# Kernel tuning notes

Hardware: AMD Instinct MI355X
Metric: run time of the kernel (lower is better)

## Reference

```python
import jax, jax.numpy as jnp
import numpy as np

DIM = 1024
NUM_HEADS = 16
HEAD_DIM = DIM // NUM_HEADS
SCALE = HEAD_DIM ** -0.5


def setup_inputs() -> dict:
    key = jax.random.key(0)
    k1, k2, k3 = jax.random.split(key, 3)
    x = jax.random.normal(k1, (4, 2048, DIM), dtype=jnp.float32)
    w_qkv = jax.random.normal(k2, (DIM, 3 * DIM), dtype=jnp.float32) * (DIM ** -0.5)
    b_qkv = jnp.zeros((3 * DIM,), dtype=jnp.float32)
    w_proj = jax.random.normal(k3, (DIM, DIM), dtype=jnp.float32) * (DIM ** -0.5)
    b_proj = jnp.zeros((DIM,), dtype=jnp.float32)
    return {"x": x, "w_qkv": w_qkv, "b_qkv": b_qkv, "w_proj": w_proj, "b_proj": b_proj}


def reference(x, w_qkv, b_qkv, w_proj, b_proj):
    b, n, c = x.shape
    qkv = x @ w_qkv + b_qkv                       # [b, n, 3*dim]
    qkv = qkv.reshape(b, n, 3, NUM_HEADS, HEAD_DIM)
    qkv = jnp.transpose(qkv, (2, 0, 3, 1, 4))     # [3, b, H, n, hd]
    q, k, v = qkv[0], qkv[1], qkv[2]
    attn = jnp.einsum("bhqd,bhkd->bhqk", q, k) * SCALE
    attn = jax.nn.softmax(attn, axis=-1)
    out = jnp.einsum("bhqk,bhkd->bhqd", attn, v)  # [b, H, n, hd]
    out = jnp.transpose(out, (0, 2, 1, 3)).reshape(b, n, c)
    return out @ w_proj + b_proj
```

## Files before the change

### kernel.cpp

```cpp
#include <hip/hip_runtime.h>
#include <hip/hip_bf16.h>

typedef unsigned short u16;
typedef __attribute__((ext_vector_type(8))) short bf16x8;
typedef __attribute__((ext_vector_type(4))) float f32x4;
typedef __attribute__((ext_vector_type(16))) float f32x16;


__device__ __forceinline__ u16 f2bf(float f) {
  union { float f; unsigned u; } v; v.f = f;
  unsigned r = v.u + 0x7fffu + ((v.u >> 16) & 1u);
  return (u16)(r >> 16);
}

#if defined(__has_builtin)
#if __has_builtin(__builtin_amdgcn_cvt_pk_bf16_f32)
#define HAS_PK_BF16 1
#endif
#endif
__device__ __forceinline__ unsigned pk2bf(float a, float b) {
#ifdef HAS_PK_BF16
  typedef __attribute__((ext_vector_type(2))) __bf16 vbf2;
  union { vbf2 v; unsigned u; } u;
  u.v = __builtin_amdgcn_cvt_pk_bf16_f32(a, b);
  return u.u;
#else
  return (unsigned)f2bf(a) | ((unsigned)f2bf(b) << 16);
#endif
}

__device__ __forceinline__ f32x4 mfma16(bf16x8 a, bf16x8 b, f32x4 c) {
  return __builtin_amdgcn_mfma_f32_16x16x32_bf16(a, b, c, 0, 0, 0);
}
__device__ __forceinline__ f32x16 mfma32(bf16x8 a, bf16x8 b, f32x16 c) {
  return __builtin_amdgcn_mfma_f32_32x32x16_bf16(a, b, c, 0, 0, 0);
}

__device__ __forceinline__ void gl_lds16(const void* g, void* l) {
  __builtin_amdgcn_global_load_lds((__attribute__((address_space(1))) void*)g,
                                   (__attribute__((address_space(3))) void*)l,
                                   16, 0, 0);
}


__global__ void cvt_f32_bf16(const float* __restrict__ in, u16* __restrict__ out, int n) {
  int i = (blockIdx.x * blockDim.x + threadIdx.x) * 4;
  if (i >= n) return;
  float4 v = *(const float4*)(in + i);
  u16 o0 = f2bf(v.x), o1 = f2bf(v.y), o2 = f2bf(v.z), o3 = f2bf(v.w);
  ushort4 o; o.x = o0; o.y = o1; o.z = o2; o.w = o3;
  *(ushort4*)(out + i) = o;
}

__global__ void transpose_cvt2(const float* __restrict__ wq, const float* __restrict__ wp,
                               u16* __restrict__ oq, u16* __restrict__ op) {
  __shared__ u16 tile[64][65];
  const int bx = blockIdx.x;
  const float* in; u16* out; int C, c0;
  if (bx < 48) { in = wq; out = oq; C = 3072; c0 = bx * 64; }
  else         { in = wp; out = op; C = 1024; c0 = (bx - 48) * 64; }
  const int R = 1024;
  int r0 = blockIdx.y * 64;
  int lc = threadIdx.x & 63, lr = threadIdx.x >> 6;
#pragma unroll
  for (int i = 0; i < 16; ++i) {
    int r = lr + i * 4;
    tile[r][lc] = f2bf(in[(size_t)(r0 + r) * C + c0 + lc]);
  }
  __syncthreads();
#pragma unroll
  for (int i = 0; i < 16; ++i) {
    int c = lr + i * 4;
    out[(size_t)(c0 + c) * R + r0 + lc] = tile[lc][c];
  }
}


struct Smem128 { u16 A0[8192]; u16 B0[16384]; u16 A1[8192]; u16 B1[16384]; };

#define LDB128(base, off) (*(const bf16x8*)((const char*)(base) + (off)))
#define ISSUE_A(dst, j, k0) \
  gl_lds16(pA + (size_t)(j) * 32768 + (k0), (dst) + (j) * 4096 + dsel)
#define ISSUE_B(dst, j, k0) \
  gl_lds16(pB + (size_t)(j) * 65536 + (k0), (dst) + (j) * 4096 + dsel)

#define KSTEP(CA, CB, NA, NB, k0n, PF)                                         \
  do {                                                                         \
    bf16x8 aL[2][2], aH[2][2], bL[2][2], bH[2][2];                             \
            \
    _Pragma("unroll") for (int mt = 0; mt < 2; ++mt) {                         \
      aL[mt][0] = LDB128(CA, aoff + mt * 2048 + cp0);                          \
      aL[mt][1] = LDB128(CA, aoff + mt * 2048 + cp1);                          \
    }                                                                          \
    _Pragma("unroll") for (int nt = 0; nt < 2; ++nt) {                         \
      bL[nt][0] = LDB128(CB, boff + nt * 2048 + cp0);                          \
      bL[nt][1] = LDB128(CB, boff + nt * 2048 + cp1);                          \
    }                                                                          \
    if (PF) { ISSUE_B(NB, 0, k0n); ISSUE_B(NB, 1, k0n); }                      \
    __builtin_amdgcn_s_setprio(1);                                             \
    _Pragma("unroll") for (int mt = 0; mt < 2; ++mt)                           \
      _Pragma("unroll") for (int nt = 0; nt < 2; ++nt) {                       \
        acc[mt][nt] = mfma16(aL[mt][0], bL[nt][0], acc[mt][nt]);               \
        acc[mt][nt] = mfma16(aL[mt][1], bL[nt][1], acc[mt][nt]);               \
      }                                                                        \
    __builtin_amdgcn_s_setprio(0);                                             \
                          \
    _Pragma("unroll") for (int nt = 0; nt < 2; ++nt) {                         \
      bH[nt][0] = LDB128(CB, boff + (nt + 2) * 2048 + cp0);                    \
      bH[nt][1] = LDB128(CB, boff + (nt + 2) * 2048 + cp1);                    \
    }                                                                          \
    if (PF) { ISSUE_B(NB, 2, k0n); ISSUE_B(NB, 3, k0n); ISSUE_A(NA, 0, k0n); } \
    __builtin_amdgcn_s_setprio(1);                                             \
    _Pragma("unroll") for (int mt = 0; mt < 2; ++mt)                           \
      _Pragma("unroll") for (int nt = 0; nt < 2; ++nt) {                       \
        acc[mt][nt + 2] = mfma16(aL[mt][0], bH[nt][0], acc[mt][nt + 2]);       \
        acc[mt][nt + 2] = mfma16(aL[mt][1], bH[nt][1], acc[mt][nt + 2]);       \
      }                                                                        \
    __builtin_amdgcn_s_setprio(0);                                             \
     \
    if (PF) asm volatile("s_waitcnt vmcnt(5)" ::: "memory");                   \
    else    asm volatile("s_waitcnt vmcnt(0)" ::: "memory");                   \
    __builtin_amdgcn_s_barrier();                                              \
    _Pragma("unroll") for (int mt = 0; mt < 2; ++mt) {                         \
      aH[mt][0] = LDB128(CA, 8192 + aoff + mt * 2048 + cp0);                   \
      aH[mt][1] = LDB128(CA, 8192 + aoff + mt * 2048 + cp1);                   \
    }                                                                          \
    if (PF) ISSUE_A(NA, 1, k0n);                                               \
    __builtin_amdgcn_s_setprio(1);                                             \
    _Pragma("unroll") for (int mt = 0; mt < 2; ++mt)                           \
      _Pragma("unroll") for (int nt = 0; nt < 2; ++nt) {                       \
        acc[mt + 2][nt + 2] = mfma16(aH[mt][0], bH[nt][0], acc[mt + 2][nt + 2]); \
        acc[mt + 2][nt + 2] = mfma16(aH[mt][1], bH[nt][1], acc[mt + 2][nt + 2]); \
      }                                                                        \
    __builtin_amdgcn_s_setprio(0);                                             \
                             \
    __builtin_amdgcn_s_setprio(1);                                             \
    _Pragma("unroll") for (int mt = 0; mt < 2; ++mt)                           \
      _Pragma("unroll") for (int nt = 0; nt < 2; ++nt) {                       \
        acc[mt + 2][nt] = mfma16(aH[mt][0], bL[nt][0], acc[mt + 2][nt]);       \
        acc[mt + 2][nt] = mfma16(aH[mt][1], bL[nt][1], acc[mt + 2][nt]);       \
      }                                                                        \
    __builtin_amdgcn_s_setprio(0);                                             \
    if (PF) asm volatile("s_waitcnt vmcnt(1)" ::: "memory");                   \
    __builtin_amdgcn_s_barrier();                                              \
  } while (0)

#define GEMM128_SETUP(Amat, Bmat)                                              \
  __shared__ Smem128 sm;                                                       \
  const int t = threadIdx.x, lane = t & 63, wave = t >> 6;                     \
  const int quad = lane >> 4, l15 = lane & 15;                                 \
  const int wm = wave >> 2, wn = wave & 3;                                     \
  const int row0 = blockIdx.x * 128, col0 = blockIdx.y * 256;                  \
  const int g = t >> 3, f0 = g + (g & 32);      \
  const int swz = (t & 7) ^ (g & 7);                                           \
  const u16* pA = (Amat) + (size_t)(row0 + f0) * 1024 + swz * 8;               \
  const u16* pB = (Bmat) + (size_t)(col0 + g) * 1024 + swz * 8;                \
  const size_t dsel = (size_t)wave * 512;                                      \
  const int rm = l15 & 7;                                                      \
  const int aoff = wm * 4096 + l15 * 128;                                      \
  const int boff = (wn * 64 + l15) * 128;                                      \
  const int cp0 = (quad ^ rm) << 4, cp1 = ((quad + 4) ^ rm) << 4;              \
  f32x4 acc[4][4] = {};                                                        \
  ISSUE_B(sm.B0, 0, 0); ISSUE_B(sm.B0, 1, 0);                                  \
  ISSUE_B(sm.B0, 2, 0); ISSUE_B(sm.B0, 3, 0);                                  \
  ISSUE_A(sm.A0, 0, 0); ISSUE_A(sm.A0, 1, 0);                                  \
  asm volatile("s_waitcnt vmcnt(1)" ::: "memory");                             \
  __builtin_amdgcn_s_barrier();                                                \
  _Pragma("unroll 1")                                                          \
  for (int kk = 0; kk < 8; ++kk) {                                             \
    KSTEP(sm.A0, sm.B0, sm.A1, sm.B1, (2 * kk + 1) * 64, 1);                   \
    KSTEP(sm.A1, sm.B1, sm.A0, sm.B0, (2 * kk + 2) * 64, (kk < 7));            \
  }


__global__ __launch_bounds__(512, 2) void gemm_qkv(
    const u16* __restrict__ A, const u16* __restrict__ Bt,
    const float* __restrict__ bias,
    u16* __restrict__ Qb, u16* __restrict__ Kb, u16* __restrict__ Vt) {
  GEMM128_SETUP(A, Bt)

  const int which = col0 >> 10;

  if (which == 2) {
    u16* Ts = ((u16*)&sm) + wave * 4096;
#pragma unroll
    for (int nt = 0; nt < 4; ++nt) {
      const int d = nt * 16 + l15;
      const float bv = bias[col0 + wn * 64 + nt * 16 + l15];
#pragma unroll
      for (int mt = 0; mt < 4; ++mt) {
        uint2 pk;
        pk.x = pk2bf(acc[mt][nt][0] + bv, acc[mt][nt][1] + bv);
        pk.y = pk2bf(acc[mt][nt][2] + bv, acc[mt][nt][3] + bv);
        *(uint2*)((char*)Ts + d * 128 +
                  (((mt * 4 + quad) ^ ((d & 7) << 1)) << 3)) = pk;
      }
    }
    const int h = ((col0 - 2048) >> 6) + wn;
    const int b_ = row0 >> 11;
    const int s0w = (row0 & 2047) + wm * 64;
    u16* vt = Vt + (size_t)(b_ * 16 + h) * 64 * 2048;
#pragma unroll
    for (int i = 0; i < 8; ++i) {
      const int d = i * 8 + (lane >> 3), c = lane & 7;
      uint4 v = *(const uint4*)((const char*)Ts + d * 128 + ((c ^ (d & 7)) << 4));
      *(uint4*)(vt + (size_t)d * 2048 + s0w + c * 8) = v;
    }
    return;
  }

  u16* dst = which == 0 ? Qb : Kb;
  const float qscale = which == 0 ? 0.1803368801111137f : 1.0f;
#pragma unroll
  for (int nt = 0; nt < 4; ++nt) {
    const int col = (col0 & 1023) + wn * 64 + nt * 16 + l15;
    const float bv = bias[col0 + wn * 64 + nt * 16 + l15];
    const int h = col >> 6, d = col & 63;
#pragma unroll
    for (int mt = 0; mt < 4; ++mt) {
#pragma unroll
      for (int r = 0; r < 4; ++r) {
        const int row = row0 + wm * 64 + mt * 16 + quad * 4 + r;
        const int bb = row >> 11, s = row & 2047;
        dst[(((size_t)bb * 16 + h) * 2048 + s) * 64 + d] =
            f2bf((acc[mt][nt][r] + bv) * qscale);
      }
    }
  }
}


__global__ __launch_bounds__(512, 2) void gemm_proj(
    const u16* __restrict__ A, const u16* __restrict__ Bt,
    const float* __restrict__ bias, float* __restrict__ C) {
  GEMM128_SETUP(A, Bt)

#pragma unroll
  for (int nt = 0; nt < 4; ++nt) {
    const int col = col0 + wn * 64 + nt * 16 + l15;
    const float bv = bias[col];
#pragma unroll
    for (int mt = 0; mt < 4; ++mt) {
#pragma unroll
      for (int r = 0; r < 4; ++r) {
        const int row = row0 + wm * 64 + mt * 16 + quad * 4 + r;
        C[(size_t)row * 1024 + col] = acc[mt][nt][r] + bv;
      }
    }
  }
}


__device__ __forceinline__ void softmax32(const f32x16& s, float& l,
                                          bf16x8& paA, bf16x8& paB) {
  unsigned D[8];
#pragma unroll
  for (int i = 0; i < 8; ++i) {
    float a = __builtin_amdgcn_exp2f(s[2 * i]);
    float b = __builtin_amdgcn_exp2f(s[2 * i + 1]);
    l += a + b;
    D[i] = pk2bf(a, b);
  }
  {
    unsigned x = D[0], x2 = D[1], y = D[2], y2 = D[3];
    asm volatile("v_permlane32_swap_b32 %0, %1" : "+v"(x), "+v"(y));
    asm volatile("v_permlane32_swap_b32 %0, %1" : "+v"(x2), "+v"(y2));
    union { unsigned u[4]; bf16x8 v; } p;
    p.u[0] = x; p.u[1] = x2; p.u[2] = y; p.u[3] = y2;
    paA = p.v;
  }
  {
    unsigned x = D[4], x2 = D[5], y = D[6], y2 = D[7];
    asm volatile("v_permlane32_swap_b32 %0, %1" : "+v"(x), "+v"(y));
    asm volatile("v_permlane32_swap_b32 %0, %1" : "+v"(x2), "+v"(y2));
    union { unsigned u[4]; bf16x8 v; } p;
    p.u[0] = x; p.u[1] = x2; p.u[2] = y; p.u[3] = y2;
    paB = p.v;
  }
}

__global__ __launch_bounds__(256, 2) void attn_kernel(
    const u16* __restrict__ Qb, const u16* __restrict__ Kb,
    const u16* __restrict__ Vt, u16* __restrict__ Ob) {
  __shared__ u16 KsA[64 * 64], KsB[64 * 64];
  __shared__ u16 VsA[64 * 64], VsB[64 * 64];
  const int bh = blockIdx.x, q0 = blockIdx.y * 256;
  const u16* Qp = Qb + (size_t)bh * 2048 * 64;
  const u16* Kp = Kb + (size_t)bh * 2048 * 64;
  const u16* Vp = Vt + (size_t)bh * 64 * 2048;
  const int t = threadIdx.x, lane = t & 63, wave = t >> 6;
  const int l31 = lane & 31, hi = lane >> 5;

  const int kr0 = t >> 3, kc0 = (t & 7) ^ (kr0 & 7);
  const int kr1 = (256 + t) >> 3, kc1 = ((256 + t) & 7) ^ (kr1 & 7);
  const u16* Kg0 = Kp + (size_t)kr0 * 64 + kc0 * 8;
  const u16* Kg1 = Kp + (size_t)kr1 * 64 + kc1 * 8;
  const u16* Vg0 = Vp + (size_t)kr0 * 2048 + kc0 * 8;
  const u16* Vg1 = Vp + (size_t)kr1 * 2048 + kc1 * 8;
  const size_t dof0 = (size_t)wave * 512;
  const size_t dof1 = 2048 + (size_t)wave * 512;

#define STAGE(Kd, Vd, key0)                                   \
  do {                                                        \
    gl_lds16(Kg0 + (size_t)(key0) * 64, (Kd) + dof0);         \
    gl_lds16(Kg1 + (size_t)(key0) * 64, (Kd) + dof1);         \
    gl_lds16(Vg0 + (key0), (Vd) + dof0);                      \
    gl_lds16(Vg1 + (key0), (Vd) + dof1);                      \
  } while (0)

  STAGE(KsA, VsA, 0);
  const u16* Qr0 = Qp + (size_t)(q0 + wave * 64 + l31) * 64 + hi * 8;
  const u16* Qr1 = Qr0 + 32 * 64;
  bf16x8 qf0[4], qf1[4];
#pragma unroll
  for (int dc = 0; dc < 4; ++dc) {
    qf0[dc] = *(const bf16x8*)(Qr0 + dc * 16);
    qf1[dc] = *(const bf16x8*)(Qr1 + dc * 16);
  }
  __syncthreads();

  const int rm = l31 & 7;
  int off[2][4];
#pragma unroll
  for (int x = 0; x < 2; ++x)
#pragma unroll
    for (int c = 0; c < 4; ++c)
      off[x][c] = x * 4096 + l31 * 128 + (((c * 2 + hi) ^ rm) << 4);

  f32x16 acc00 = {}, acc01 = {}, acc10 = {}, acc11 = {};
  float l0 = 0.f, l1 = 0.f;

#define TILE(Ks, Vs)                                                          \
  do {                                                                        \
    _Pragma("unroll")                                                         \
    for (int kh = 0; kh < 2; ++kh) {                                          \
      f32x16 s0 = {}, s1 = {};                                                \
      __builtin_amdgcn_s_setprio(1);                                          \
      _Pragma("unroll")                                                       \
      for (int dc = 0; dc < 4; ++dc) {                                        \
        bf16x8 kf = *(const bf16x8*)((const char*)(Ks) + off[kh][dc]);        \
        s0 = mfma32(kf, qf0[dc], s0);                                         \
        s1 = mfma32(kf, qf1[dc], s1);                                         \
      }                                                                       \
      __builtin_amdgcn_s_setprio(0);                                          \
      bf16x8 pa00, pa01, pa10, pa11;                                          \
      softmax32(s0, l0, pa00, pa01);                                          \
      softmax32(s1, l1, pa10, pa11);                                          \
      __builtin_amdgcn_s_setprio(1);                                          \
      _Pragma("unroll")                                                       \
      for (int ci = 0; ci < 2; ++ci) {                                        \
        const int c = 2 * kh + ci;                                            \
        bf16x8 vlo = *(const bf16x8*)((const char*)(Vs) + off[0][c]);         \
        bf16x8 vhiv = *(const bf16x8*)((const char*)(Vs) + off[1][c]);        \
        bf16x8 pa0 = ci ? pa01 : pa00;                                        \
        bf16x8 pa1 = ci ? pa11 : pa10;                                        \
        acc00 = mfma32(pa0, vlo, acc00);                                      \
        acc01 = mfma32(pa0, vhiv, acc01);                                     \
        acc10 = mfma32(pa1, vlo, acc10);                                      \
        acc11 = mfma32(pa1, vhiv, acc11);                                     \
      }                                                                       \
      __builtin_amdgcn_s_setprio(0);                                          \
    }                                                                         \
  } while (0)

#pragma unroll 1
  for (int kt2 = 0; kt2 < 16; ++kt2) {
    const int kt = kt2 * 2;
    STAGE(KsB, VsB, (kt + 1) * 64);
    TILE(KsA, VsA);
    __syncthreads();
    if (kt2 < 15) STAGE(KsA, VsA, (kt + 2) * 64);
    TILE(KsB, VsB);
    __syncthreads();
  }
#undef TILE
#undef STAGE

  l0 += __shfl_xor(l0, 32);
  l1 += __shfl_xor(l1, 32);
  float inv0 = 1.f / l0, inv1 = 1.f / l1;

  const int b_ = bh >> 4, h = bh & 15;
  const int qw = q0 + wave * 64;
#pragma unroll
  for (int r = 0; r < 16; ++r) {
    const int ql = (r & 3) + 8 * (r >> 2) + 4 * hi;
    float iv0 = __shfl(inv0, ql);
    float iv1 = __shfl(inv1, ql);
    size_t base0 = ((size_t)b_ * 2048 + qw + ql) * 1024 + h * 64;
    size_t base1 = base0 + (size_t)32 * 1024;
    Ob[base0 + l31] = f2bf(acc00[r] * iv0);
    Ob[base0 + 32 + l31] = f2bf(acc01[r] * iv0);
    Ob[base1 + l31] = f2bf(acc10[r] * iv1);
    Ob[base1 + 32 + l31] = f2bf(acc11[r] * iv1);
  }
}


extern "C" void kernel_launch(void* const* d_in, const int* in_sizes, int n_in,
                              void* d_out, int out_size, void* d_ws, size_t ws_size,
                              hipStream_t stream) {
  const float* x      = (const float*)d_in[0];
  const float* w_qkv  = (const float*)d_in[1];
  const float* b_qkv  = (const float*)d_in[2];
  const float* w_proj = (const float*)d_in[3];
  const float* b_proj = (const float*)d_in[4];
  float* out = (float*)d_out;
  char* ws = (char*)d_ws;

  u16* xb    = (u16*)(ws);
  u16* wqkvt = (u16*)(ws + 16777216);
  u16* wprjt = (u16*)(ws + 23068672);
  u16* Qb    = (u16*)(ws + 25165824);
  u16* Kb    = (u16*)(ws + 41943040);
  u16* Vt    = (u16*)(ws + 58720256);
  u16* Ob    = xb;
  if (ws_size < 92274688u) return;

  cvt_f32_bf16<<<8192, 256, 0, stream>>>(x, xb, 8388608);
  transpose_cvt2<<<dim3(64, 16), 256, 0, stream>>>(w_qkv, w_proj, wqkvt, wprjt);
  gemm_qkv<<<dim3(64, 12), 512, 0, stream>>>(xb, wqkvt, b_qkv, Qb, Kb, Vt);
  attn_kernel<<<dim3(64, 8), 256, 0, stream>>>(Qb, Kb, Vt, Ob);
  gemm_proj<<<dim3(64, 4), 512, 0, stream>>>(Ob, wprjt, b_proj, out);
}
```

Before: 253.4 us.

## Split attention key range across two wave groups and reduce partials in LDS

The attention block grows from 256 to 512 threads. Two groups of four waves each handle half of the 2048 keys for the same 256 queries, each with its own double-buffered K/V LDS tiles. At the end, the second group writes its partial accumulators and row sums into the reused LDS buffers and exits, and the first group adds them in before normalising and storing. This doubles the waves per block and halves the serial key loop to raise occupancy and hide latency. The cost is extra LDS, a register spill-over risk under the new launch bounds, and an LDS reduction step. The merge adds partials without any max rescaling, so it is only correct if the softmax uses a shared fixed offset rather than a per-half running max.

```diff
diff --git a/kernel.cpp b/kernel.cpp
--- a/kernel.cpp
+++ b/kernel.cpp
@@ -279,26 +279,32 @@
   }
 }
 
-__global__ __launch_bounds__(256, 2) void attn_kernel(
+__global__ __launch_bounds__(512, 4) void attn_kernel(
     const u16* __restrict__ Qb, const u16* __restrict__ Kb,
     const u16* __restrict__ Vt, u16* __restrict__ Ob) {
-  __shared__ u16 KsA[64 * 64], KsB[64 * 64];
-  __shared__ u16 VsA[64 * 64], VsB[64 * 64];
+  __shared__ u16 KsA[2][4096], KsB[2][4096];
+  __shared__ u16 VsA[2][4096], VsB[2][4096];
+  __shared__ float lbuf[4][2][64];
   const int bh = blockIdx.x, q0 = blockIdx.y * 256;
   const u16* Qp = Qb + (size_t)bh * 2048 * 64;
   const u16* Kp = Kb + (size_t)bh * 2048 * 64;
   const u16* Vp = Vt + (size_t)bh * 64 * 2048;
   const int t = threadIdx.x, lane = t & 63, wave = t >> 6;
+  const int wl = wave & 3, half = wave >> 2;
   const int l31 = lane & 31, hi = lane >> 5;
 
-  const int kr0 = t >> 3, kc0 = (t & 7) ^ (kr0 & 7);
-  const int kr1 = (256 + t) >> 3, kc1 = ((256 + t) & 7) ^ (kr1 & 7);
-  const u16* Kg0 = Kp + (size_t)kr0 * 64 + kc0 * 8;
-  const u16* Kg1 = Kp + (size_t)kr1 * 64 + kc1 * 8;
-  const u16* Vg0 = Vp + (size_t)kr0 * 2048 + kc0 * 8;
-  const u16* Vg1 = Vp + (size_t)kr1 * 2048 + kc1 * 8;
-  const size_t dof0 = (size_t)wave * 512;
-  const size_t dof1 = 2048 + (size_t)wave * 512;
+  const int tl = t & 255;
+  const int kr0 = tl >> 3, kc0 = (tl & 7) ^ (kr0 & 7);
+  const int kr1 = (256 + tl) >> 3, kc1 = ((256 + tl) & 7) ^ (kr1 & 7);
+  const u16* Kg0 = Kp + (size_t)(half * 1024 + kr0) * 64 + kc0 * 8;
+  const u16* Kg1 = Kp + (size_t)(half * 1024 + kr1) * 64 + kc1 * 8;
+  const u16* Vg0 = Vp + (size_t)kr0 * 2048 + half * 1024 + kc0 * 8;
+  const u16* Vg1 = Vp + (size_t)kr1 * 2048 + half * 1024 + kc1 * 8;
+  const size_t dof0 = (size_t)wl * 512;
+  const size_t dof1 = 2048 + (size_t)wl * 512;
+
+  u16* Ksa = KsA[half]; u16* Ksb = KsB[half];
+  u16* Vsa = VsA[half]; u16* Vsb = VsB[half];
 
 #define STAGE(Kd, Vd, key0)                                   \
   do {                                                        \
@@ -308,8 +314,8 @@
     gl_lds16(Vg1 + (key0), (Vd) + dof1);                      \
   } while (0)
 
-  STAGE(KsA, VsA, 0);
-  const u16* Qr0 = Qp + (size_t)(q0 + wave * 64 + l31) * 64 + hi * 8;
+  STAGE(Ksa, Vsa, 0);
+  const u16* Qr0 = Qp + (size_t)(q0 + wl * 64 + l31) * 64 + hi * 8;
   const u16* Qr1 = Qr0 + 32 * 64;
   bf16x8 qf0[4], qf1[4];
 #pragma unroll
@@ -364,24 +370,48 @@
   } while (0)
 
 #pragma unroll 1
-  for (int kt2 = 0; kt2 < 16; ++kt2) {
+  for (int kt2 = 0; kt2 < 8; ++kt2) {
     const int kt = kt2 * 2;
-    STAGE(KsB, VsB, (kt + 1) * 64);
-    TILE(KsA, VsA);
+    STAGE(Ksb, Vsb, (kt + 1) * 64);
+    TILE(Ksa, Vsa);
     __syncthreads();
-    if (kt2 < 15) STAGE(KsA, VsA, (kt + 2) * 64);
-    TILE(KsB, VsB);
+    if (kt2 < 7) STAGE(Ksa, Vsa, (kt + 2) * 64);
+    TILE(Ksb, Vsb);
     __syncthreads();
   }
 #undef TILE
 #undef STAGE
+
+  float* cb = (float*)(wl == 0 ? KsA[0] : wl == 1 ? KsB[0] : wl == 2 ? VsA[0] : VsB[0]);
+  if (half == 1) {
+#pragma unroll
+    for (int i = 0; i < 16; ++i) {
+      cb[i * 64 + lane] = acc00[i];
+      cb[(16 + i) * 64 + lane] = acc01[i];
+      cb[(32 + i) * 64 + lane] = acc10[i];
+      cb[(48 + i) * 64 + lane] = acc11[i];
+    }
+    lbuf[wl][0][lane] = l0;
+    lbuf[wl][1][lane] = l1;
+  }
+  __syncthreads();
+  if (half == 1) return;
+#pragma unroll
+  for (int i = 0; i < 16; ++i) {
+    acc00[i] += cb[i * 64 + lane];
+    acc01[i] += cb[(16 + i) * 64 + lane];
+    acc10[i] += cb[(32 + i) * 64 + lane];
+    acc11[i] += cb[(48 + i) * 64 + lane];
+  }
+  l0 += lbuf[wl][0][lane];
+  l1 += lbuf[wl][1][lane];
 
   l0 += __shfl_xor(l0, 32);
   l1 += __shfl_xor(l1, 32);
   float inv0 = 1.f / l0, inv1 = 1.f / l1;
 
   const int b_ = bh >> 4, h = bh & 15;
-  const int qw = q0 + wave * 64;
+  const int qw = q0 + wl * 64;
 #pragma unroll
   for (int r = 0; r < 16; ++r) {
     const int ql = (r & 3) + 8 * (r >> 2) + 4 * hi;
@@ -420,6 +450,6 @@
   cvt_f32_bf16<<<8192, 256, 0, stream>>>(x, xb, 8388608);
   transpose_cvt2<<<dim3(64, 16), 256, 0, stream>>>(w_qkv, w_proj, wqkvt, wprjt);
   gemm_qkv<<<dim3(64, 12), 512, 0, stream>>>(xb, wqkvt, b_qkv, Qb, Kb, Vt);
-  attn_kernel<<<dim3(64, 8), 256, 0, stream>>>(Qb, Kb, Vt, Ob);
+  attn_kernel<<<dim3(64, 8), 512, 0, stream>>>(Qb, Kb, Vt, Ob);
   gemm_proj<<<dim3(64, 4), 512, 0, stream>>>(Ob, wprjt, b_proj, out);
 }
```

After: 580.1 us. 2.29x slower.
